# Kernel tuning notes

Measured on AMD Instinct MI355X. Metric: run time of the kernel, lower is better.

The kernel has to match this reference:

```python
import jax, jax.numpy as jnp
import numpy as np

DECAY = 0.99
EPS = 1e-05


def setup_inputs() -> dict:
    key = jax.random.key(0)
    k1, k2 = jax.random.split(key)
    B, D, T, K = 8, 256, 2048, 8192
    x = jax.random.normal(k1, (B, D, T), dtype=jnp.float32)
    # xavier_uniform init for the [K, D] codebook
    bound = float(np.sqrt(6.0 / (K + D)))
    embeddings = jax.random.uniform(k2, (K, D), dtype=jnp.float32,
                                    minval=-bound, maxval=bound)
    return {"x": x, "embeddings": embeddings}


def reference(x, embeddings):
    # x: [B, D, T]; embeddings: [K, D]. Training-mode forward (EMA update, STE).
    B, D, T = x.shape
    K = embeddings.shape[0]

    vq_in = jnp.transpose(x, (0, 2, 1))          # [B, T, D]
    flatten = vq_in.reshape(-1, D)               # [N, D], N = B*T

    # get_code_indices: squared-L2 distances via expansion + argmin
    distances = (jnp.sum(flatten ** 2, axis=1, keepdims=True)
                 + jnp.sum(embeddings ** 2, axis=1)
                 - 2.0 * flatten @ embeddings.T)  # [N, K]
    encoding_indices = jnp.argmin(distances, axis=1)  # [N]

    # quantize: codebook gather (uses pre-update embeddings, as in torch)
    vq_out = embeddings[encoding_indices].reshape(vq_in.shape)  # [B, T, D]

    # --- EMA codebook update (no_grad block; first step: counter=1, hidden=0) ---
    # one-hot column sums == bincount; one-hot^T @ flatten == segment_sum
    cluster_size = jax.ops.segment_sum(
        jnp.ones_like(encoding_indices, dtype=flatten.dtype),
        encoding_indices, num_segments=K)                       # [K]
    dw = jax.ops.segment_sum(flatten, encoding_indices, num_segments=K)  # [K, D]

    one_m_decay = 1.0 - DECAY
    bias_corr = 1.0 - DECAY ** 1  # counter == 1
    ema_cs = (cluster_size * one_m_decay) / bias_corr           # == cluster_size
    ema_dw = (dw * one_m_decay) / bias_corr                     # == dw

    n = jnp.sum(ema_cs)
    ema_cs = (ema_cs + EPS) / (n + K * EPS) * n
    new_embeddings = ema_dw / ema_cs[:, None]                   # [K, D]

    # straight-through estimator
    vq_out_st = vq_in + jax.lax.stop_gradient(vq_out - vq_in)   # [B, T, D]

    quantized = jnp.transpose(vq_out_st, (0, 2, 1))             # [B, D, T]
    vq_in_bdt = jnp.transpose(vq_in, (0, 2, 1))                 # [B, D, T]
    return (quantized, vq_in_bdt, jax.lax.stop_gradient(quantized),
            new_embeddings)
```

## Files before the change

kernel.cpp:

```cpp
#include <hip/hip_runtime.h>
#include <stdint.h>

#define B_ 8
#define D_ 256
#define T_ 2048
#define K_ 8192
#define N_ (B_*T_)

typedef __attribute__((ext_vector_type(8))) __bf16 bf16x8;
typedef __attribute__((ext_vector_type(4))) __bf16 bf16x4;
typedef __attribute__((ext_vector_type(2))) __bf16 bf16x2;
typedef __attribute__((ext_vector_type(4))) float f32x4;


__global__ __launch_bounds__(256) void prep_e_kernel(const float* __restrict__ E,
                                                     __bf16* __restrict__ E2,
                                                     float* __restrict__ sse) {
    int row  = blockIdx.x * 4 + (threadIdx.x >> 6);
    int lane = threadIdx.x & 63;
    float4 v = *(const float4*)(E + (size_t)row * D_ + lane * 4);
    __bf16 h0 = (__bf16)v.x, h1 = (__bf16)v.y, h2 = (__bf16)v.z, h3 = (__bf16)v.w;
    __bf16 l0 = (__bf16)(v.x - (float)h0), l1 = (__bf16)(v.y - (float)h1);
    __bf16 l2 = (__bf16)(v.z - (float)h2), l3 = (__bf16)(v.w - (float)h3);
    bf16x4 hv = {h0, h1, h2, h3};
    bf16x4 lv = {l0, l1, l2, l3};
    int p0  = lane >> 4;
    int col = (lane & 15) * 4;
    *(bf16x4*)(E2 + ((size_t)(p0    ) * K_ + row) * 64 + col) = lv;
    *(bf16x4*)(E2 + ((size_t)(p0 + 4) * K_ + row) * 64 + col) = hv;
    float s = __fadd_rn(__fadd_rn(__fmul_rn(v.x, v.x), __fmul_rn(v.y, v.y)),
                        __fadd_rn(__fmul_rn(v.z, v.z), __fmul_rn(v.w, v.w)));
    #pragma unroll
    for (int off = 32; off > 0; off >>= 1) s += __shfl_down(s, off);
    if (lane == 0) sse[row] = s;
}

__global__ __launch_bounds__(256) void prep_x_kernel(const float* __restrict__ x,
                                                     __bf16* __restrict__ X2,
                                                     float* __restrict__ ssx) {
    __shared__ float tile[64][65];
    __shared__ float part[64][4];
    int bidx = blockIdx.x;
    int b    = bidx >> 7;
    int dblk = (bidx >> 5) & 3;
    int tblk = bidx & 31;
    int d0 = dblk * 64, t0 = tblk * 64;
    const float* xp = x + (size_t)b * D_ * T_;
    {
        int tl = threadIdx.x & 63, th = threadIdx.x >> 6;
        float s = 0.f;
        #pragma unroll
        for (int i = 0; i < 16; i++) {
            int d = i * 4 + th;
            float v = xp[(size_t)(d0 + d) * T_ + t0 + tl];
            tile[d][tl] = v;
            s = __fadd_rn(s, __fmul_rn(v, v));
        }
        part[tl][th] = s;
    }
    __syncthreads();
    if (threadIdx.x < 64) {
        float tot = __fadd_rn(__fadd_rn(__fadd_rn(part[threadIdx.x][0],
                    part[threadIdx.x][1]), part[threadIdx.x][2]), part[threadIdx.x][3]);
        atomicAdd(ssx + b * T_ + t0 + threadIdx.x, tot);
    }
    {
        int dp = (threadIdx.x & 31) * 2, th = threadIdx.x >> 5;
        #pragma unroll
        for (int i = 0; i < 8; i++) {
            int t = i * 8 + th;
            float v0 = tile[dp][t], v1 = tile[dp + 1][t];
            __bf16 h0 = (__bf16)v0, h1 = (__bf16)v1;
            __bf16 q0 = (__bf16)(v0 - (float)h0), q1 = (__bf16)(v1 - (float)h1);
            size_t n = (size_t)b * T_ + t0 + t;
            bf16x2 hv = {h0, h1};
            bf16x2 lv = {q0, q1};
            *(bf16x2*)(X2 + ((size_t)(dblk    ) * N_ + n) * 64 + dp) = hv;
            *(bf16x2*)(X2 + ((size_t)(dblk + 4) * N_ + n) * 64 + dp) = lv;
        }
    }
}


#define STAGE_A(kt, half, buf) do {                                             \
    const int pkt_ = ((kt) >= 8) ? (kt) - 4 : (kt);                             \
    const char* gp_ = (const char*)A2 + ((size_t)pkt_ * K_ + c0 + (half) * 128) * 128; \
    __bf16* lp_ = smem + ((buf) * 2 + (half)) * 8192;                           \
    __builtin_amdgcn_global_load_lds((const __attribute__((address_space(1))) void*)(gp_ + s1), \
        (__attribute__((address_space(3))) void*)(lp_ + wb1), 16, 0, 0);        \
    __builtin_amdgcn_global_load_lds((const __attribute__((address_space(1))) void*)(gp_ + s1 + 8192), \
        (__attribute__((address_space(3))) void*)(lp_ + wb2), 16, 0, 0);        \
  } while (0)

#define STAGE_B(kt, half, buf) do {                                             \
    const int pkt_ = (kt) & 7;                                                  \
    const char* gp_ = (const char*)B2 + ((size_t)pkt_ * N_ + r0 + (half) * 128) * 128; \
    __bf16* lp_ = smem + 32768 + ((buf) * 2 + (half)) * 8192;                   \
    __builtin_amdgcn_global_load_lds((const __attribute__((address_space(1))) void*)(gp_ + s1), \
        (__attribute__((address_space(3))) void*)(lp_ + wb1), 16, 0, 0);        \
    __builtin_amdgcn_global_load_lds((const __attribute__((address_space(1))) void*)(gp_ + s1 + 8192), \
        (__attribute__((address_space(3))) void*)(lp_ + wb2), 16, 0, 0);        \
  } while (0)

#define VMW(N) do { asm volatile("s_waitcnt vmcnt(" #N ")" ::: "memory");       \
                    __builtin_amdgcn_sched_barrier(0); } while (0)
#define NOPW ((void)0)

#define LOAD_A(DST, PA)                                                          \
    _Pragma("unroll")                                                            \
    for (int kk = 0; kk < 2; kk++) {                                             \
      _Pragma("unroll")                                                          \
      for (int i = 0; i < 4; i++) {                                              \
        int row_ = wm * 64 + i * 16 + (l & 15);                                  \
        int byt_ = (row_ * 128 + (kk * 4 + (l >> 4)) * 16) ^ ((row_ & 7) << 4);  \
        DST[kk][i] = *(const bf16x8*)((const char*)(PA) + byt_);                 \
      }                                                                          \
    }

#define LOAD_B(DST, PB)                                                          \
    _Pragma("unroll")                                                            \
    for (int kk = 0; kk < 2; kk++) {                                             \
      _Pragma("unroll")                                                          \
      for (int j = 0; j < 2; j++) {                                              \
        int row_ = wn * 32 + j * 16 + (l & 15);                                  \
        int byt_ = (row_ * 128 + (kk * 4 + (l >> 4)) * 16) ^ ((row_ & 7) << 4);  \
        DST[kk][j] = *(const bf16x8*)((const char*)(PB) + byt_);                 \
      }                                                                          \
    }

#define MFMA16(H, G, AF, BF)                                                     \
    _Pragma("unroll")                                                            \
    for (int kk = 0; kk < 2; kk++)                                               \
      _Pragma("unroll")                                                          \
      for (int i = 0; i < 4; i++)                                                \
        _Pragma("unroll")                                                        \
        for (int j = 0; j < 2; j++)                                              \
          acc[(H) * 4 + i][(G) * 2 + j] = __builtin_amdgcn_mfma_f32_16x16x32_bf16( \
              AF[kk][i], BF[kk][j], acc[(H) * 4 + i][(G) * 2 + j], 0, 0, 0)

#define PHX(LOADS, STAGE_STMT, H, G, AF, BF, WAIT_STMT) do {                     \
    LOADS;                                                                       \
    STAGE_STMT;                                                                  \
    __builtin_amdgcn_s_barrier();                                                \
    asm volatile("s_waitcnt lgkmcnt(0)" ::: "memory");                           \
    __builtin_amdgcn_sched_barrier(0);                                           \
    __builtin_amdgcn_s_setprio(1);                                               \
    MFMA16(H, G, AF, BF);                                                        \
    __builtin_amdgcn_s_setprio(0);                                               \
    WAIT_STMT;                                                                   \
    __builtin_amdgcn_s_barrier();                                                \
    __builtin_amdgcn_sched_barrier(0);                                           \
  } while (0)

#define KTILE(bufi, S1, W1, S2, W2, S3, W3, S4, W4) do {                         \
    const __bf16* paL_ = smem + ((bufi) * 2 + 0) * 8192;                         \
    const __bf16* paH_ = smem + ((bufi) * 2 + 1) * 8192;                         \
    const __bf16* pbL_ = smem + 32768 + ((bufi) * 2 + 0) * 8192;                 \
    const __bf16* pbH_ = smem + 32768 + ((bufi) * 2 + 1) * 8192;                 \
    bf16x8 af_[2][4], b0_[2][2], b1_[2][2];                                      \
    PHX({ LOAD_A(af_, paL_); LOAD_B(b0_, pbL_); }, S1, 0, 0, af_, b0_, W1);      \
    PHX({ LOAD_B(b1_, pbH_); },                    S2, 0, 1, af_, b1_, W2);      \
    PHX({ LOAD_A(af_, paH_); },                    S3, 1, 1, af_, b1_, W3);      \
    PHX({ ; },                                     S4, 1, 0, af_, b0_, W4);      \
  } while (0)

__global__ __launch_bounds__(512, 2) void dist_kernel(
    const __bf16* __restrict__ A2, const __bf16* __restrict__ B2,
    const float* __restrict__ ssx, const float* __restrict__ sse,
    unsigned long long* __restrict__ best)
{
    extern __shared__ __bf16 smem[];

    const int tid = threadIdx.x;
    const int l   = tid & 63;
    const int w   = tid >> 6;
    const int wm  = w >> 2;
    const int wn  = w & 3;

    const int bid = blockIdx.x;
    const int xq  = bid & 7;
    const int i_  = bid >> 3;
    const int c0  = (xq * 4 + (i_ & 3)) * 256;
    const int r0  = (i_ >> 2) * 256;

    const int o1  = tid * 16;
    const int s1  = o1 ^ (((tid >> 3) & 7) << 4);
    const int wb1 = w * 512;
    const int wb2 = w * 512 + 4096;

    f32x4 acc[8][4];
    #pragma unroll
    for (int i = 0; i < 8; i++)
        #pragma unroll
        for (int j = 0; j < 4; j++) acc[i][j] = (f32x4)0.f;

    STAGE_A(0, 0, 0); STAGE_B(0, 0, 0);
    STAGE_A(0, 1, 0); STAGE_B(0, 1, 0);
    STAGE_A(1, 0, 1); STAGE_B(1, 0, 1);
    VMW(8);
    __builtin_amdgcn_s_barrier();
    __builtin_amdgcn_sched_barrier(0);

    #pragma unroll 1
    for (int it = 0; it < 5; it++) {
        const int tX = 2 * it;
        KTILE(0, STAGE_A(tX + 1, 1, 1), VMW(6),
                 STAGE_B(tX + 1, 1, 1), NOPW,
                 STAGE_A(tX + 2, 0, 0), NOPW,
                 STAGE_B(tX + 2, 0, 0), VMW(8));
        KTILE(1, STAGE_A(tX + 2, 1, 0), VMW(6),
                 STAGE_B(tX + 2, 1, 0), NOPW,
                 STAGE_A(tX + 3, 0, 1), NOPW,
                 STAGE_B(tX + 3, 0, 1), VMW(8));
    }
    KTILE(0, STAGE_A(11, 1, 1), VMW(6),
             STAGE_B(11, 1, 1), NOPW,
             NOPW, NOPW,
             NOPW, VMW(4));
    KTILE(1, NOPW, VMW(0),
             NOPW, NOPW,
             NOPW, NOPW,
             NOPW, NOPW);

    #pragma unroll
    for (int g = 0; g < 2; g++) {
        #pragma unroll
        for (int j = 0; j < 2; j++) {
            int xrow = r0 + g * 128 + wn * 32 + j * 16 + (l & 15);
            float sx = ssx[xrow];
            unsigned long long m = ~0ull;
            #pragma unroll
            for (int h = 0; h < 2; h++) {
                #pragma unroll
                for (int i = 0; i < 4; i++) {
                    int cbase = c0 + h * 128 + wm * 64 + i * 16 + (l >> 4) * 4;
                    float4 sc = *(const float4*)(sse + cbase);
                    f32x4 a = acc[h * 4 + i][g * 2 + j];
                    float d0 = (sx + sc.x) - 2.0f * a[0];
                    float d1 = (sx + sc.y) - 2.0f * a[1];
                    float d2 = (sx + sc.z) - 2.0f * a[2];
                    float d3 = (sx + sc.w) - 2.0f * a[3];
                    unsigned long long p;
                    p = ((unsigned long long)__float_as_uint(d0) << 32) | (unsigned)(cbase + 0);
                    if (p < m) m = p;
                    p = ((unsigned long long)__float_as_uint(d1) << 32) | (unsigned)(cbase + 1);
                    if (p < m) m = p;
                    p = ((unsigned long long)__float_as_uint(d2) << 32) | (unsigned)(cbase + 2);
                    if (p < m) m = p;
                    p = ((unsigned long long)__float_as_uint(d3) << 32) | (unsigned)(cbase + 3);
                    if (p < m) m = p;
                }
            }
            unsigned long long o;
            o = __shfl_xor(m, 16); if (o < m) m = o;
            o = __shfl_xor(m, 32); if (o < m) m = o;
            if ((l >> 4) == 0) atomicMin(best + xrow, m);
        }
    }
}

__global__ __launch_bounds__(256) void scatter_kernel(
    const float* __restrict__ x, const float* __restrict__ E,
    const unsigned long long* __restrict__ best,
    float* __restrict__ out, int* __restrict__ cs, float* __restrict__ dw)
{
    __shared__ float tx[64][68];
    __shared__ float te[64][68];
    __shared__ int sidx[64];

    const int blk = blockIdx.x;
    const int b   = blk >> 5;
    const int t0  = (blk & 31) * 64;
    const int tid = threadIdx.x;
    const int n0  = b * T_ + t0;

    if (tid < 64) {
        int ix = (int)(best[n0 + tid] & 0xffffffffu);
        sidx[tid] = ix;
        atomicAdd(cs + ix, 1);
    }
    __syncthreads();

    const int t4   = (tid & 15) * 4;
    const int dg   = tid >> 4;
    const int l    = tid & 63;
    const int w    = tid >> 6;
    const int nsub = l >> 4;
    const int dl4  = (l & 15) * 4;

    float* o0 = out;
    float* o1 = out + (size_t)N_ * D_;
    float* o2 = out + 2 * (size_t)N_ * D_;

    for (int dc = 0; dc < 4; dc++) {
        const int d0 = dc * 64;
        #pragma unroll
        for (int r = 0; r < 4; r++) {
            int d = r * 16 + dg;
            size_t gi = ((size_t)(b * D_ + d0 + d)) * T_ + t0 + t4;
            float4 v = *(const float4*)(x + gi);
            *(float4*)&tx[d][t4] = v;
            *(float4*)(o1 + gi) = v;
        }
        #pragma unroll
        for (int i = 0; i < 4; i++) {
            int nl  = w * 16 + i * 4 + nsub;
            int row = sidx[nl];
            float4 ev = *(const float4*)(E + (size_t)row * D_ + d0 + dl4);
            te[dl4 + 0][nl] = ev.x;
            te[dl4 + 1][nl] = ev.y;
            te[dl4 + 2][nl] = ev.z;
            te[dl4 + 3][nl] = ev.w;
        }
        __syncthreads();
        #pragma unroll
        for (int r = 0; r < 4; r++) {
            int d = r * 16 + dg;
            float4 v = *(const float4*)&te[d][t4];
            size_t gi = ((size_t)(b * D_ + d0 + d)) * T_ + t0 + t4;
            *(float4*)(o0 + gi) = v;
            *(float4*)(o2 + gi) = v;
        }
        #pragma unroll
        for (int i = 0; i < 16; i++) {
            int nl = w * 16 + i;
            atomicAdd(dw + (size_t)sidx[nl] * D_ + d0 + l, tx[l][nl]);
        }
        __syncthreads();
    }
}

__global__ __launch_bounds__(256) void finalize_kernel(
    const int* __restrict__ cs, const float* __restrict__ dw,
    float* __restrict__ out3)
{
    int k = blockIdx.x;
    int d = threadIdx.x;
    const float C = 0.00999999977648258209228515625f;
    float c   = (float)cs[k];
    float ecs = (c * C) / C;
    float edw = (dw[(size_t)k * D_ + d] * C) / C;
    float n = 16384.0f;
    float denom = (ecs + 1e-5f) / (n + (float)K_ * 1e-5f) * n;
    out3[(size_t)k * D_ + d] = edw / denom;
}

extern "C" void kernel_launch(void* const* d_in, const int* in_sizes, int n_in,
                              void* d_out, int out_size, void* d_ws, size_t ws_size,
                              hipStream_t stream) {
    const float* x = (const float*)d_in[0];
    const float* E = (const float*)d_in[1];
    float* out = (float*)d_out;

    char* ws = (char*)d_ws;
    unsigned long long* best = (unsigned long long*)(ws);
    int*   cs  = (int*)  (ws + 131072);
    float* dw  = (float*)(ws + 163840);
    float* sse = (float*)(ws + 8552448);
    float* ssx = (float*)(ws + 8585216);

    __bf16* X2 = (__bf16*)out;
    __bf16* E2 = (__bf16*)(out + 2 * (size_t)N_ * D_);

    hipMemsetAsync(best, 0xFF, (size_t)N_ * 8, stream);
    hipMemsetAsync(cs, 0, 8650752 - 131072, stream);

    hipFuncSetAttribute((const void*)dist_kernel,
                        hipFuncAttributeMaxDynamicSharedMemorySize, 131072);

    prep_e_kernel<<<K_ / 4, 256, 0, stream>>>(E, E2, sse);
    prep_x_kernel<<<1024, 256, 0, stream>>>(x, X2, ssx);
    dist_kernel<<<2048, 512, 131072, stream>>>(E2, X2, ssx, sse, best);
    scatter_kernel<<<256, 256, 0, stream>>>(x, E, best, out, cs, dw);
    finalize_kernel<<<K_, 256, 0, stream>>>(cs, dw, out + 3 * (size_t)N_ * D_);
}
```

Measured before the change: 229.3 us.

## Merge last two MFMA phases and drop explicit lgkmcnt wait per phase

Restructures the per-K-tile pipeline from four barrier-delimited phases to three by merging the last two MFMA groups and their staging loads into one phase. It also removes the explicit s_waitcnt lgkmcnt(0) before MFMAs and moves the sched_barrier ahead of the workgroup barrier, letting the compiler insert finer-grained LDS waits. The aim is to cut barrier and wait overhead per tile. The risk is less interleaving of global loads with compute, and changed register pressure.

```diff
diff --git a/kernel.cpp b/kernel.cpp
--- a/kernel.cpp
+++ b/kernel.cpp
@@ -138,30 +138,31 @@
           acc[(H) * 4 + i][(G) * 2 + j] = __builtin_amdgcn_mfma_f32_16x16x32_bf16( \
               AF[kk][i], BF[kk][j], acc[(H) * 4 + i][(G) * 2 + j], 0, 0, 0)
 
-#define PHX(LOADS, STAGE_STMT, H, G, AF, BF, WAIT_STMT) do {                     \
+#define PHX(LOADS, STAGE_STMT, MFMAS, WAIT_STMT) do {                            \
     LOADS;                                                                       \
     STAGE_STMT;                                                                  \
+    __builtin_amdgcn_sched_barrier(0);                                           \
     __builtin_amdgcn_s_barrier();                                                \
-    asm volatile("s_waitcnt lgkmcnt(0)" ::: "memory");                           \
-    __builtin_amdgcn_sched_barrier(0);                                           \
     __builtin_amdgcn_s_setprio(1);                                               \
-    MFMA16(H, G, AF, BF);                                                        \
+    MFMAS;                                                                       \
     __builtin_amdgcn_s_setprio(0);                                               \
     WAIT_STMT;                                                                   \
     __builtin_amdgcn_s_barrier();                                                \
     __builtin_amdgcn_sched_barrier(0);                                           \
   } while (0)
 
-#define KTILE(bufi, S1, W1, S2, W2, S3, W3, S4, W4) do {                         \
+#define KTILE(bufi, S1, W1, S2, S3, S4, W3) do {                                 \
     const __bf16* paL_ = smem + ((bufi) * 2 + 0) * 8192;                         \
     const __bf16* paH_ = smem + ((bufi) * 2 + 1) * 8192;                         \
     const __bf16* pbL_ = smem + 32768 + ((bufi) * 2 + 0) * 8192;                 \
     const __bf16* pbH_ = smem + 32768 + ((bufi) * 2 + 1) * 8192;                 \
     bf16x8 af_[2][4], b0_[2][2], b1_[2][2];                                      \
-    PHX({ LOAD_A(af_, paL_); LOAD_B(b0_, pbL_); }, S1, 0, 0, af_, b0_, W1);      \
-    PHX({ LOAD_B(b1_, pbH_); },                    S2, 0, 1, af_, b1_, W2);      \
-    PHX({ LOAD_A(af_, paH_); },                    S3, 1, 1, af_, b1_, W3);      \
-    PHX({ ; },                                     S4, 1, 0, af_, b0_, W4);      \
+    PHX({ LOAD_A(af_, paL_); LOAD_B(b0_, pbL_); }, S1,                           \
+        MFMA16(0, 0, af_, b0_), W1);                                             \
+    PHX({ LOAD_B(b1_, pbH_); }, S2,                                              \
+        MFMA16(0, 1, af_, b1_), NOPW);                                           \
+    PHX({ LOAD_A(af_, paH_); }, { S3; S4; },                                     \
+        { MFMA16(1, 1, af_, b1_); MFMA16(1, 0, af_, b0_); }, W3);                \
   } while (0)
 
 __global__ __launch_bounds__(512, 2) void dist_kernel(
@@ -205,21 +206,21 @@
     for (int it = 0; it < 5; it++) {
         const int tX = 2 * it;
         KTILE(0, STAGE_A(tX + 1, 1, 1), VMW(6),
-                 STAGE_B(tX + 1, 1, 1), NOPW,
-                 STAGE_A(tX + 2, 0, 0), NOPW,
+                 STAGE_B(tX + 1, 1, 1),
+                 STAGE_A(tX + 2, 0, 0),
                  STAGE_B(tX + 2, 0, 0), VMW(8));
         KTILE(1, STAGE_A(tX + 2, 1, 0), VMW(6),
-                 STAGE_B(tX + 2, 1, 0), NOPW,
-                 STAGE_A(tX + 3, 0, 1), NOPW,
+                 STAGE_B(tX + 2, 1, 0),
+                 STAGE_A(tX + 3, 0, 1),
                  STAGE_B(tX + 3, 0, 1), VMW(8));
     }
     KTILE(0, STAGE_A(11, 1, 1), VMW(6),
-             STAGE_B(11, 1, 1), NOPW,
-             NOPW, NOPW,
+             STAGE_B(11, 1, 1),
+             NOPW,
              NOPW, VMW(4));
     KTILE(1, NOPW, VMW(0),
-             NOPW, NOPW,
-             NOPW, NOPW,
+             NOPW,
+             NOPW,
              NOPW, NOPW);
 
     #pragma unroll
```

Result: no change. 229.0 us (-0.1%).
